# Optimization experiments

Measured on AMD Instinct MI355X. Metric: run time of the kernel, lower is better.

The kernel has to match this reference:

```python
import jax, jax.numpy as jnp
import numpy as np

B, S, D, V, H, L = 2, 64, 1024, 32000, 8, 2
HD = D // H

def setup_inputs():
    key = jax.random.key(0)
    ks = jax.random.split(key, 12)
    w = lambda k, shp: jax.random.normal(k, shp, jnp.float32) * 0.02
    return {
        "embedded_answer": jax.random.normal(ks[0], (B, S, D), jnp.float32),
        "sa_in_w": w(ks[1], (L, 3 * D, D)), "sa_in_b": jnp.zeros((L, 3 * D), jnp.float32),
        "sa_out_w": w(ks[2], (L, D, D)), "sa_out_b": jnp.zeros((L, D), jnp.float32),
        "ca_in_w": w(ks[3], (L, 3 * D, D)), "ca_in_b": jnp.zeros((L, 3 * D), jnp.float32),
        "ca_out_w": w(ks[4], (L, D, D)), "ca_out_b": jnp.zeros((L, D), jnp.float32),
        "ff1_w": w(ks[5], (L, 4 * D, D)), "ff1_b": jnp.zeros((L, 4 * D), jnp.float32),
        "ff2_w": w(ks[6], (L, D, 4 * D)), "ff2_b": jnp.zeros((L, D), jnp.float32),
        "ln_w": jnp.ones((L, 3, D), jnp.float32), "ln_b": jnp.zeros((L, 3, D), jnp.float32),
        "out_w": w(ks[7], (V, D)), "out_b": jnp.zeros((V,), jnp.float32),
        "temp_w": w(ks[8], (1, D)), "temp_b": jnp.zeros((1,), jnp.float32),
        "len_w": w(ks[9], (1, D)), "len_b": jnp.zeros((1,), jnp.float32),
        "style_w": w(ks[10], (D, D)), "style_b": jnp.zeros((D,), jnp.float32),
        "num_steps": 8,
    }

def _ln(x, w, b, eps=1e-5):
    m = x.mean(-1, keepdims=True)
    v = ((x - m) ** 2).mean(-1, keepdims=True)
    return (x - m) * jax.lax.rsqrt(v + eps) * w + b

def _mha(q_in, kv_in, in_w, in_b, ow, ob):
    wq, wk, wv = jnp.split(in_w, 3, 0)
    bq, bk, bv = jnp.split(in_b, 3, 0)
    q = (q_in @ wq.T + bq).reshape(q_in.shape[0], q_in.shape[1], H, HD)
    k = (kv_in @ wk.T + bk).reshape(kv_in.shape[0], kv_in.shape[1], H, HD)
    v = (kv_in @ wv.T + bv).reshape(kv_in.shape[0], kv_in.shape[1], H, HD)
    a = jax.nn.softmax(jnp.einsum('bqhd,bkhd->bhqk', q, k) * (HD ** -0.5), axis=-1)
    o = jnp.einsum('bhqk,bkhd->bqhd', a, v).reshape(q_in.shape)
    return o @ ow.T + ob

def _decode(x, mem, l, p):
    # post-LN torch TransformerDecoderLayer (relu FFN, no masks, eval/no dropout)
    x = _ln(x + _mha(x, x, p['sa_in_w'][l], p['sa_in_b'][l], p['sa_out_w'][l], p['sa_out_b'][l]), p['ln_w'][l, 0], p['ln_b'][l, 0])
    x = _ln(x + _mha(x, mem, p['ca_in_w'][l], p['ca_in_b'][l], p['ca_out_w'][l], p['ca_out_b'][l]), p['ln_w'][l, 1], p['ln_b'][l, 1])
    h = jax.nn.relu(x @ p['ff1_w'][l].T + p['ff1_b'][l]) @ p['ff2_w'][l].T + p['ff2_b'][l]
    return _ln(x + h, p['ln_w'][l, 2], p['ln_b'][l, 2])

def reference(embedded_answer, sa_in_w, sa_in_b, sa_out_w, sa_out_b, ca_in_w, ca_in_b, ca_out_w, ca_out_b, ff1_w, ff1_b, ff2_w, ff2_b, ln_w, ln_b, out_w, out_b, temp_w, temp_b, len_w, len_b, style_w, style_b, num_steps):
    p = dict(sa_in_w=sa_in_w, sa_in_b=sa_in_b, sa_out_w=sa_out_w, sa_out_b=sa_out_b,
             ca_in_w=ca_in_w, ca_in_b=ca_in_b, ca_out_w=ca_out_w, ca_out_b=ca_out_b,
             ff1_w=ff1_w, ff1_b=ff1_b, ff2_w=ff2_w, ff2_b=ff2_b, ln_w=ln_w, ln_b=ln_b)
    # control_generation (per-batch mean temperature / mean style vector)
    temp = jax.nn.sigmoid(embedded_answer @ temp_w.T + temp_b).mean(axis=(1, 2))[:, None]  # [B,1]
    _length_factor = jax.nn.sigmoid(embedded_answer @ len_w.T + len_b)  # drives static num_steps
    style = (embedded_answer @ style_w.T + style_b).mean(axis=1, keepdims=True)  # [B,1,D]
    cur = embedded_answer
    skey = jax.random.key(42)
    toks, lgs = [], []
    for t in range(num_steps):  # static unrolled decode loop; full recompute (no KV cache), as original
        h = cur
        for l in range(L):
            h = _decode(h, embedded_answer, l, p)
        logits_last = ((h + style)[:, -1, :] @ out_w.T + out_b) / temp  # [B,V]
        nt = jax.random.categorical(jax.random.fold_in(skey, t), logits_last)  # == softmax+multinomial
        toks.append(nt)
        lgs.append(logits_last)
        cur = jnp.concatenate([cur, out_w[nt][:, None, :]], axis=1)  # re-embed via output weight rows
    return jnp.stack(toks, 1), jnp.stack(lgs, 1)
```

## Files before the change

kernel.cpp:

```cpp
#include <hip/hip_runtime.h>
#include <stdint.h>

__host__ __device__ inline void threefry2x32(uint32_t k0, uint32_t k1,
                                             uint32_t x0, uint32_t x1,
                                             uint32_t* o0, uint32_t* o1) {
  uint32_t ks2 = 0x1BD11BDAu ^ k0 ^ k1;
  x0 += k0; x1 += k1;
#define TF_R(x, r) (((x) << (r)) | ((x) >> (32 - (r))))
#define TF_ROUND(r) { x0 += x1; x1 = TF_R(x1, r); x1 ^= x0; }
  TF_ROUND(13) TF_ROUND(15) TF_ROUND(26) TF_ROUND(6)
  x0 += k1; x1 += ks2 + 1u;
  TF_ROUND(17) TF_ROUND(29) TF_ROUND(16) TF_ROUND(24)
  x0 += ks2; x1 += k0 + 2u;
  TF_ROUND(13) TF_ROUND(15) TF_ROUND(26) TF_ROUND(6)
  x0 += k0; x1 += k1 + 3u;
  TF_ROUND(17) TF_ROUND(29) TF_ROUND(16) TF_ROUND(24)
  x0 += k1; x1 += ks2 + 4u;
  TF_ROUND(13) TF_ROUND(15) TF_ROUND(26) TF_ROUND(6)
  x0 += ks2; x1 += k0 + 5u;
  *o0 = x0; *o1 = x1;
#undef TF_ROUND
#undef TF_R
}

__device__ __forceinline__ float wave_sum(float v) {
#pragma unroll
  for (int o = 32; o > 0; o >>= 1) v += __shfl_xor(v, o, 64);
  return v;
}
__device__ __forceinline__ float wave_max(float v) {
#pragma unroll
  for (int o = 32; o > 0; o >>= 1) v = fmaxf(v, __shfl_xor(v, o, 64));
  return v;
}

__global__ __launch_bounds__(256) void gemm2_kernel(
    const float* __restrict__ X, long long xbs, int ldx,
    const float* __restrict__ W, int ldw,
    const float* __restrict__ bias,
    float* __restrict__ out, long long obs, int ldo,
    int St, int M, int N, int K32, int relu, int partial) {
  __shared__ __align__(16) float Xl[2][32][68];
  __shared__ __align__(16) float Wl[2][32][68];
  const int tid = threadIdx.x;
  const int m0 = blockIdx.x * 64;
  const int n0 = blockIdx.y * 64;
  const long long kbase = (long long)blockIdx.z * K32 * 32;
  const int mi = tid >> 4;
  const int ni = tid & 15;
  const int lr = tid >> 3;
  const int lc = (tid & 7) * 4;

  const int mA = m0 + lr, mB = m0 + lr + 32;
  const float* xpA = nullptr;
  const float* xpB = nullptr;
  if (mA < M) {
    int b = mA / St, s = mA - b * St;
    xpA = X + (long long)b * xbs + (long long)s * ldx + kbase + lc;
  }
  if (mB < M) {
    int b = mB / St, s = mB - b * St;
    xpB = X + (long long)b * xbs + (long long)s * ldx + kbase + lc;
  }
  const float* wpA = W + (long long)(n0 + lr) * ldw + kbase + lc;
  const float* wpB = W + (long long)(n0 + lr + 32) * ldw + kbase + lc;

  float4 xA = xpA ? *(const float4*)xpA : make_float4(0.f, 0.f, 0.f, 0.f);
  float4 xB = xpB ? *(const float4*)xpB : make_float4(0.f, 0.f, 0.f, 0.f);
  float4 wA = *(const float4*)wpA;
  float4 wB = *(const float4*)wpB;

  float acc[4][4];
#pragma unroll
  for (int i = 0; i < 4; ++i)
#pragma unroll
    for (int j = 0; j < 4; ++j) acc[i][j] = 0.f;

  Xl[0][lc + 0][lr] = xA.x; Xl[0][lc + 1][lr] = xA.y;
  Xl[0][lc + 2][lr] = xA.z; Xl[0][lc + 3][lr] = xA.w;
  Xl[0][lc + 0][lr + 32] = xB.x; Xl[0][lc + 1][lr + 32] = xB.y;
  Xl[0][lc + 2][lr + 32] = xB.z; Xl[0][lc + 3][lr + 32] = xB.w;
  Wl[0][lc + 0][lr] = wA.x; Wl[0][lc + 1][lr] = wA.y;
  Wl[0][lc + 2][lr] = wA.z; Wl[0][lc + 3][lr] = wA.w;
  Wl[0][lc + 0][lr + 32] = wB.x; Wl[0][lc + 1][lr + 32] = wB.y;
  Wl[0][lc + 2][lr + 32] = wB.z; Wl[0][lc + 3][lr + 32] = wB.w;
  __syncthreads();

  for (int i = 0; i < K32; ++i) {
    if (i + 1 < K32) {
      int off = (i + 1) * 32;
      xA = xpA ? *(const float4*)(xpA + off) : make_float4(0.f, 0.f, 0.f, 0.f);
      xB = xpB ? *(const float4*)(xpB + off) : make_float4(0.f, 0.f, 0.f, 0.f);
      wA = *(const float4*)(wpA + off);
      wB = *(const float4*)(wpB + off);
    }
    const int cur = i & 1;
#pragma unroll
    for (int kk = 0; kk < 32; ++kk) {
      float4 xv = *(const float4*)&Xl[cur][kk][mi * 4];
      float4 wv = *(const float4*)&Wl[cur][kk][ni * 4];
      float xa[4] = {xv.x, xv.y, xv.z, xv.w};
      float wa[4] = {wv.x, wv.y, wv.z, wv.w};
#pragma unroll
      for (int a = 0; a < 4; ++a)
#pragma unroll
        for (int c = 0; c < 4; ++c) acc[a][c] = fmaf(xa[a], wa[c], acc[a][c]);
    }
    if (i + 1 < K32) {
      __syncthreads();
      const int nxt = cur ^ 1;
      Xl[nxt][lc + 0][lr] = xA.x; Xl[nxt][lc + 1][lr] = xA.y;
      Xl[nxt][lc + 2][lr] = xA.z; Xl[nxt][lc + 3][lr] = xA.w;
      Xl[nxt][lc + 0][lr + 32] = xB.x; Xl[nxt][lc + 1][lr + 32] = xB.y;
      Xl[nxt][lc + 2][lr + 32] = xB.z; Xl[nxt][lc + 3][lr + 32] = xB.w;
      Wl[nxt][lc + 0][lr] = wA.x; Wl[nxt][lc + 1][lr] = wA.y;
      Wl[nxt][lc + 2][lr] = wA.z; Wl[nxt][lc + 3][lr] = wA.w;
      Wl[nxt][lc + 0][lr + 32] = wB.x; Wl[nxt][lc + 1][lr + 32] = wB.y;
      Wl[nxt][lc + 2][lr + 32] = wB.z; Wl[nxt][lc + 3][lr + 32] = wB.w;
      __syncthreads();
    }
  }

  const int n = n0 + ni * 4;
  if (partial) {
    float* base = out + (long long)blockIdx.z * M * ldo;
#pragma unroll
    for (int i = 0; i < 4; ++i) {
      int m = m0 + mi * 4 + i;
      if (m >= M) continue;
      *(float4*)(base + (long long)m * ldo + n) =
          make_float4(acc[i][0], acc[i][1], acc[i][2], acc[i][3]);
    }
  } else {
    float4 bv = *(const float4*)(bias + n);
#pragma unroll
    for (int i = 0; i < 4; ++i) {
      int m = m0 + mi * 4 + i;
      if (m >= M) continue;
      int b = m / St, s = m - b * St;
      float4 o;
      o.x = acc[i][0] + bv.x; o.y = acc[i][1] + bv.y;
      o.z = acc[i][2] + bv.z; o.w = acc[i][3] + bv.w;
      if (relu) {
        o.x = fmaxf(o.x, 0.f); o.y = fmaxf(o.y, 0.f);
        o.z = fmaxf(o.z, 0.f); o.w = fmaxf(o.w, 0.f);
      }
      *(float4*)(out + (long long)b * obs + (long long)s * ldo + n) = o;
    }
  }
}

__global__ __launch_bounds__(256) void epi_kernel(
    const float* __restrict__ P, int splits, int M, int N,
    const float* __restrict__ bias,
    const float* __restrict__ res, long long rbs, int ldr,
    const float* __restrict__ lnw, const float* __restrict__ lnb,
    float* __restrict__ out, long long obs, int ldo, int St, int relu) {
  __shared__ float red[4];
  const int m = blockIdx.x;
  const int b = m / St, s = m - b * St;
  const int n = blockIdx.y * 1024 + threadIdx.x * 4;
  const float* pr = P + (long long)m * N + n;
  float4 v = *(const float4*)pr;
  for (int sp = 1; sp < splits; ++sp) {
    float4 w2 = *(const float4*)(pr + (long long)sp * M * N);
    v.x += w2.x; v.y += w2.y; v.z += w2.z; v.w += w2.w;
  }
  float4 bv = *(const float4*)(bias + n);
  v.x += bv.x; v.y += bv.y; v.z += bv.z; v.w += bv.w;
  if (res) {
    float4 rv = *(const float4*)(res + (long long)b * rbs + (long long)s * ldr + n);
    v.x += rv.x; v.y += rv.y; v.z += rv.z; v.w += rv.w;
  }
  if (relu) {
    v.x = fmaxf(v.x, 0.f); v.y = fmaxf(v.y, 0.f);
    v.z = fmaxf(v.z, 0.f); v.w = fmaxf(v.w, 0.f);
  }
  if (lnw) {
    const int tid = threadIdx.x;
    float sum = wave_sum(v.x + v.y + v.z + v.w);
    int wid = tid >> 6;
    if ((tid & 63) == 0) red[wid] = sum;
    __syncthreads();
    float mean = (red[0] + red[1] + red[2] + red[3]) * (1.f / 1024.f);
    float4 d;
    d.x = v.x - mean; d.y = v.y - mean; d.z = v.z - mean; d.w = v.w - mean;
    float s2 = wave_sum(d.x * d.x + d.y * d.y + d.z * d.z + d.w * d.w);
    __syncthreads();
    if ((tid & 63) == 0) red[wid] = s2;
    __syncthreads();
    float var = (red[0] + red[1] + red[2] + red[3]) * (1.f / 1024.f);
    float inv = rsqrtf(var + 1e-5f);
    float4 wv = *(const float4*)(lnw + tid * 4);
    float4 lb = *(const float4*)(lnb + tid * 4);
    v.x = d.x * inv * wv.x + lb.x;
    v.y = d.y * inv * wv.y + lb.y;
    v.z = d.z * inv * wv.z + lb.z;
    v.w = d.w * inv * wv.w + lb.w;
  }
  *(float4*)(out + (long long)b * obs + (long long)s * ldo + n) = v;
}

__global__ __launch_bounds__(64) void attn_kernel(
    const float* __restrict__ Qp, int q_rs, long long q_bs,
    const float* __restrict__ Kp, int k_rs, long long k_bs,
    const float* __restrict__ Vp, int v_rs, long long v_bs,
    float* __restrict__ Op, int o_rs, long long o_bs,
    int Sq, int Skv) {
  const int lane = threadIdx.x;
  int bid = blockIdx.x;
  int b = bid / (8 * Sq);
  int rr = bid - b * 8 * Sq;
  int h = rr / Sq;
  int sq = rr - h * Sq;
  const float* qrow = Qp + (long long)b * q_bs + (long long)sq * q_rs + h * 128;
  float q0 = qrow[lane], q1 = qrow[lane + 64];
  __shared__ float sc[72];
  const float* kb = Kp + (long long)b * k_bs + h * 128;
  for (int sk = 0; sk < Skv; ++sk) {
    const float* kr = kb + (long long)sk * k_rs;
    float p = fmaf(q0, kr[lane], q1 * kr[lane + 64]);
    p = wave_sum(p);
    if (lane == 0) sc[sk] = p * 0.08838834764831845f;
  }
  __syncthreads();
  float m = -3.4e38f;
  for (int i = lane; i < Skv; i += 64) m = fmaxf(m, sc[i]);
  m = wave_max(m);
  float ssum = 0.f;
  for (int i = lane; i < Skv; i += 64) {
    float e = expf(sc[i] - m);
    sc[i] = e;
    ssum += e;
  }
  ssum = wave_sum(ssum);
  __syncthreads();
  float o0 = 0.f, o1 = 0.f;
  const float* vb = Vp + (long long)b * v_bs + h * 128;
  for (int sk = 0; sk < Skv; ++sk) {
    float w = sc[sk];
    const float* vr = vb + (long long)sk * v_rs;
    o0 = fmaf(w, vr[lane], o0);
    o1 = fmaf(w, vr[lane + 64], o1);
  }
  float inv = 1.f / ssum;
  float* orow = Op + (long long)b * o_bs + (long long)sq * o_rs + h * 128;
  orow[lane] = o0 * inv;
  orow[lane + 64] = o1 * inv;
}

__global__ __launch_bounds__(256) void copy_cur_kernel(
    const float* __restrict__ emb, float* __restrict__ cur) {
  int idx = blockIdx.x * 256 + threadIdx.x;
  int b = idx >> 16;
  int r = idx & 65535;
  cur[(long long)b * 73728 + r] = emb[idx];
}

__global__ __launch_bounds__(256) void xmean_kernel(
    const float* __restrict__ emb, float* __restrict__ xmean) {
  int idx = blockIdx.x * 256 + threadIdx.x;
  int b = idx >> 10, d = idx & 1023;
  float s = 0.f;
  for (int ss = 0; ss < 64; ++ss) s += emb[b * 65536 + ss * 1024 + d];
  xmean[idx] = s * (1.f / 64.f);
}

__global__ __launch_bounds__(256) void temp_kernel(
    const float* __restrict__ emb, const float* __restrict__ tw,
    const float* __restrict__ tb, float* __restrict__ tempv) {
  __shared__ float red[4];
  int b = blockIdx.x;
  int wid = threadIdx.x >> 6, lane = threadIdx.x & 63;
  float acc = 0.f;
  for (int s = wid; s < 64; s += 4) {
    const float* x = emb + b * 65536 + s * 1024;
    float p = 0.f;
#pragma unroll
    for (int it = 0; it < 4; ++it) {
      float4 xv = *(const float4*)(x + it * 256 + lane * 4);
      float4 wv = *(const float4*)(tw + it * 256 + lane * 4);
      p += xv.x * wv.x + xv.y * wv.y + xv.z * wv.z + xv.w * wv.w;
    }
    p = wave_sum(p);
    acc += 1.f / (1.f + expf(-(p + tb[0])));
  }
  if (lane == 0) red[wid] = acc;
  __syncthreads();
  if (threadIdx.x == 0)
    tempv[b] = (red[0] + red[1] + red[2] + red[3]) * (1.f / 64.f);
}

__global__ __launch_bounds__(256) void style_kernel(
    const float* __restrict__ xmean, const float* __restrict__ sw,
    const float* __restrict__ sb, float* __restrict__ stylev) {
  int wid = threadIdx.x >> 6, lane = threadIdx.x & 63;
  int d = blockIdx.x * 4 + wid;
  const float* wr = sw + (long long)d * 1024;
  float a0 = 0.f, a1 = 0.f;
#pragma unroll
  for (int it = 0; it < 4; ++it) {
    float4 wv = *(const float4*)(wr + it * 256 + lane * 4);
    float4 x0 = *(const float4*)(xmean + it * 256 + lane * 4);
    float4 x1 = *(const float4*)(xmean + 1024 + it * 256 + lane * 4);
    a0 += wv.x * x0.x + wv.y * x0.y + wv.z * x0.z + wv.w * x0.w;
    a1 += wv.x * x1.x + wv.y * x1.y + wv.z * x1.z + wv.w * x1.w;
  }
  a0 = wave_sum(a0);
  a1 = wave_sum(a1);
  if (lane == 0) {
    stylev[d] = a0 + sb[d];
    stylev[1024 + d] = a1 + sb[d];
  }
}

__global__ __launch_bounds__(256) void z_kernel(
    const float* __restrict__ A, const float* __restrict__ stylev,
    float* __restrict__ z, int St) {
  int idx = blockIdx.x * 256 + threadIdx.x;
  int b = idx >> 10, d = idx & 1023;
  z[idx] = A[(long long)b * 73728 + (long long)(St - 1) * 1024 + d] + stylev[idx];
}

__global__ __launch_bounds__(256) void logits_kernel(
    const float* __restrict__ z, const float* __restrict__ Wo,
    const float* __restrict__ bo, const float* __restrict__ tempv,
    float* __restrict__ outl, int t) {
  int wid = threadIdx.x >> 6, lane = threadIdx.x & 63;
  int n = blockIdx.x * 4 + wid;
  const float* wr = Wo + (long long)n * 1024;
  float a0 = 0.f, a1 = 0.f;
#pragma unroll
  for (int it = 0; it < 4; ++it) {
    float4 wv = *(const float4*)(wr + it * 256 + lane * 4);
    float4 z0 = *(const float4*)(z + it * 256 + lane * 4);
    float4 z1 = *(const float4*)(z + 1024 + it * 256 + lane * 4);
    a0 += wv.x * z0.x + wv.y * z0.y + wv.z * z0.z + wv.w * z0.w;
    a1 += wv.x * z1.x + wv.y * z1.y + wv.z * z1.z + wv.w * z1.w;
  }
  a0 = wave_sum(a0);
  a1 = wave_sum(a1);
  if (lane == 0) {
    float bb = bo[n];
    outl[(long long)(0 * 8 + t) * 32000 + n] = (a0 + bb) / tempv[0];
    outl[(long long)(1 * 8 + t) * 32000 + n] = (a1 + bb) / tempv[1];
  }
}

__global__ __launch_bounds__(1024) void sample_kernel(
    const float* __restrict__ logits, float* __restrict__ tok_f,
    int* __restrict__ tok_i, uint32_t fk0, uint32_t fk1, int t) {
  int b = blockIdx.x;
  const float* lg = logits + (long long)(b * 8 + t) * 32000;
  float best = -3.4e38f;
  int bi = 0x7fffffff;
  for (int n = threadIdx.x; n < 32000; n += 1024) {
    uint32_t r0, r1;
    threefry2x32(fk0, fk1, 0u, (uint32_t)(b * 32000 + n), &r0, &r1);
    uint32_t bits = (r0 ^ r1) >> 9;
    float u = __uint_as_float(0x3f800000u | bits) - 1.0f;
    if (u < 1.1754944e-38f) u = 1.1754944e-38f;
    float g = -logf(-logf(u));
    float val = lg[n] + g;
    if (val > best) { best = val; bi = n; }
  }
  __shared__ float bv[1024];
  __shared__ int bix[1024];
  bv[threadIdx.x] = best;
  bix[threadIdx.x] = bi;
  __syncthreads();
  for (int s = 512; s > 0; s >>= 1) {
    if (threadIdx.x < s) {
      float ov = bv[threadIdx.x + s];
      int oi = bix[threadIdx.x + s];
      if (ov > bv[threadIdx.x] ||
          (ov == bv[threadIdx.x] && oi < bix[threadIdx.x])) {
        bv[threadIdx.x] = ov;
        bix[threadIdx.x] = oi;
      }
    }
    __syncthreads();
  }
  if (threadIdx.x == 0) {
    tok_i[b] = bix[0];
    tok_f[b * 8 + t] = (float)bix[0];
  }
}

__global__ __launch_bounds__(256) void append_kernel(
    const float* __restrict__ Wo, const int* __restrict__ tok_i,
    float* __restrict__ cur, int St) {
  int idx = blockIdx.x * 256 + threadIdx.x;
  int b = idx >> 10, d = idx & 1023;
  cur[(long long)b * 73728 + (long long)St * 1024 + d] =
      Wo[(long long)tok_i[b] * 1024 + d];
}

static inline void g2(hipStream_t st, const float* X, long long xbs, int ldx,
                      const float* W, int ldw, const float* bias, float* out,
                      long long obs, int ldo, int St, int M, int N, int K,
                      int splits, int relu, int partial) {
  dim3 grid((unsigned)((M + 63) / 64), (unsigned)(N / 64), (unsigned)splits);
  gemm2_kernel<<<grid, 256, 0, st>>>(X, xbs, ldx, W, ldw, bias, out, obs, ldo,
                                     St, M, N, K / (32 * splits), relu,
                                     partial);
}

static inline void epi(hipStream_t st, const float* P, int splits, int M,
                       int N, const float* bias, const float* res,
                       long long rbs, int ldr, const float* lnw,
                       const float* lnb, float* out, long long obs, int ldo,
                       int St, int relu) {
  dim3 grid((unsigned)M, (unsigned)(N / 1024));
  epi_kernel<<<grid, 256, 0, st>>>(P, splits, M, N, bias, res, rbs, ldr, lnw,
                                   lnb, out, obs, ldo, St, relu);
}

extern "C" void kernel_launch(void* const* d_in, const int* in_sizes, int n_in,
                              void* d_out, int out_size, void* d_ws,
                              size_t ws_size, hipStream_t stream) {
  const float* emb = (const float*)d_in[0];
  const float* sa_in_w = (const float*)d_in[1];
  const float* sa_in_b = (const float*)d_in[2];
  const float* sa_out_w = (const float*)d_in[3];
  const float* sa_out_b = (const float*)d_in[4];
  const float* ca_in_w = (const float*)d_in[5];
  const float* ca_in_b = (const float*)d_in[6];
  const float* ca_out_w = (const float*)d_in[7];
  const float* ca_out_b = (const float*)d_in[8];
  const float* ff1_w = (const float*)d_in[9];
  const float* ff1_b = (const float*)d_in[10];
  const float* ff2_w = (const float*)d_in[11];
  const float* ff2_b = (const float*)d_in[12];
  const float* ln_w = (const float*)d_in[13];
  const float* ln_b = (const float*)d_in[14];
  const float* out_w = (const float*)d_in[15];
  const float* out_b = (const float*)d_in[16];
  const float* temp_w = (const float*)d_in[17];
  const float* temp_b = (const float*)d_in[18];
  const float* style_w = (const float*)d_in[21];
  const float* style_b = (const float*)d_in[22];

  float* ws = (float*)d_ws;
  float* cur = ws;
  float* A = cur + 2 * 72 * 1024;
  float* Qb = A + 2 * 72 * 1024;
  float* Tb = Qb + 2 * 72 * 3072;
  float* T2 = Tb + 2 * 72 * 1024;
  float* Fb = T2 + 2 * 72 * 1024;
  float* cakv = Fb + 2 * 72 * 4096;
  float* Pp = cakv + 2 * 2 * 64 * 2048;
  float* xmean = Pp + 1310720;
  float* stylev = xmean + 2048;
  float* tempv = stylev + 2048;
  float* zbuf = tempv + 16;
  int* toki = (int*)(zbuf + 2048);

  float* toks_out = (float*)d_out;
  float* logits_out = toks_out + 16;

  copy_cur_kernel<<<512, 256, 0, stream>>>(emb, cur);
  xmean_kernel<<<8, 256, 0, stream>>>(emb, xmean);
  temp_kernel<<<2, 256, 0, stream>>>(emb, temp_w, temp_b, tempv);
  style_kernel<<<256, 256, 0, stream>>>(xmean, style_w, style_b, stylev);
  for (int l = 0; l < 2; ++l) {
    g2(stream, emb, 64 * 1024, 1024,
       ca_in_w + (size_t)(l * 3072 + 1024) * 1024, 1024,
       ca_in_b + l * 3072 + 1024, cakv + (size_t)l * 2 * 64 * 2048, 64 * 2048,
       2048, 64, 128, 2048, 1024, 1, 0, 0);
  }

  for (int t = 0; t < 8; ++t) {
    int St = 64 + t;
    int M = 2 * St;
    for (int l = 0; l < 2; ++l) {
      const float* P0 = (l == 0) ? cur : A;
      g2(stream, P0, 72 * 1024, 1024, sa_in_w + (size_t)l * 3072 * 1024, 1024,
         nullptr, Pp, 0, 3072, St, M, 3072, 1024, 2, 0, 1);
      epi(stream, Pp, 2, M, 3072, sa_in_b + l * 3072, nullptr, 0, 0, nullptr,
          nullptr, Qb, 72 * 3072, 3072, St, 0);
      attn_kernel<<<2 * 8 * St, 64, 0, stream>>>(
          Qb, 3072, 72 * 3072, Qb + 1024, 3072, 72 * 3072, Qb + 2048, 3072,
          72 * 3072, Tb, 1024, 72 * 1024, St, St);
      g2(stream, Tb, 72 * 1024, 1024, sa_out_w + (size_t)l * 1024 * 1024, 1024,
         nullptr, Pp, 0, 1024, St, M, 1024, 1024, 4, 0, 1);
      epi(stream, Pp, 4, M, 1024, sa_out_b + l * 1024, P0, 72 * 1024, 1024,
          ln_w + (l * 3 + 0) * 1024, ln_b + (l * 3 + 0) * 1024, A, 72 * 1024,
          1024, St, 0);
      g2(stream, A, 72 * 1024, 1024, ca_in_w + (size_t)l * 3072 * 1024, 1024,
         nullptr, Pp, 0, 1024, St, M, 1024, 1024, 4, 0, 1);
      epi(stream, Pp, 4, M, 1024, ca_in_b + l * 3072, nullptr, 0, 0, nullptr,
          nullptr, T2, 72 * 1024, 1024, St, 0);
      attn_kernel<<<2 * 8 * St, 64, 0, stream>>>(
          T2, 1024, 72 * 1024, cakv + (size_t)l * 2 * 64 * 2048, 2048,
          64 * 2048, cakv + (size_t)l * 2 * 64 * 2048 + 1024, 2048, 64 * 2048,
          Tb, 1024, 72 * 1024, St, 64);
      g2(stream, Tb, 72 * 1024, 1024, ca_out_w + (size_t)l * 1024 * 1024, 1024,
         nullptr, Pp, 0, 1024, St, M, 1024, 1024, 4, 0, 1);
      epi(stream, Pp, 4, M, 1024, ca_out_b + l * 1024, A, 72 * 1024, 1024,
          ln_w + (l * 3 + 1) * 1024, ln_b + (l * 3 + 1) * 1024, A, 72 * 1024,
          1024, St, 0);
      g2(stream, A, 72 * 1024, 1024, ff1_w + (size_t)l * 4096 * 1024, 1024,
         nullptr, Pp, 0, 4096, St, M, 4096, 1024, 2, 0, 1);
      epi(stream, Pp, 2, M, 4096, ff1_b + l * 4096, nullptr, 0, 0, nullptr,
          nullptr, Fb, 72 * 4096, 4096, St, 1);
      g2(stream, Fb, 72 * 4096, 4096, ff2_w + (size_t)l * 1024 * 4096, 4096,
         nullptr, Pp, 0, 1024, St, M, 1024, 4096, 8, 0, 1);
      epi(stream, Pp, 8, M, 1024, ff2_b + l * 1024, A, 72 * 1024, 1024,
          ln_w + (l * 3 + 2) * 1024, ln_b + (l * 3 + 2) * 1024, A, 72 * 1024,
          1024, St, 0);
    }
    z_kernel<<<8, 256, 0, stream>>>(A, stylev, zbuf, St);
    logits_kernel<<<8000, 256, 0, stream>>>(zbuf, out_w, out_b, tempv,
                                            logits_out, t);
    uint32_t fk0, fk1;
    threefry2x32(0u, 42u, 0u, (uint32_t)t, &fk0, &fk1);
    sample_kernel<<<2, 1024, 0, stream>>>(logits_out, toks_out, toki, fk0, fk1,
                                          t);
    append_kernel<<<8, 256, 0, stream>>>(out_w, toki, cur, St);
  }
}
```

Baseline: 5.627 ms.

## Fuse epilogues into GEMMs, attention, logits and sampling to cut launches

Removes separate epilogue launches. The QKV and FF1 projections now run unsplit and write bias (and ReLU) directly from the GEMM, and the cross-attention Q projection uses a 2-way split whose two partials plus bias are summed inside the attention kernel. The z kernel is folded into the logits kernel, and the token-append kernel is folded into the sampling kernel. This cuts roughly 5 launches per layer-step and some intermediate traffic, at the cost of less split-K parallelism for the unsplit GEMMs.

```diff
diff --git a/kernel.cpp b/kernel.cpp
--- a/kernel.cpp
+++ b/kernel.cpp
@@ -203,6 +203,8 @@
 
 __global__ __launch_bounds__(64) void attn_kernel(
     const float* __restrict__ Qp, int q_rs, long long q_bs,
+    const float* __restrict__ Qp2,
+    const float* __restrict__ qbias,
     const float* __restrict__ Kp, int k_rs, long long k_bs,
     const float* __restrict__ Vp, int v_rs, long long v_bs,
     float* __restrict__ Op, int o_rs, long long o_bs,
@@ -215,6 +217,13 @@
   int sq = rr - h * Sq;
   const float* qrow = Qp + (long long)b * q_bs + (long long)sq * q_rs + h * 128;
   float q0 = qrow[lane], q1 = qrow[lane + 64];
+  if (Qp2) {
+    const float* q2 = Qp2 + (long long)b * q_bs + (long long)sq * q_rs + h * 128;
+    q0 += q2[lane]; q1 += q2[lane + 64];
+  }
+  if (qbias) {
+    q0 += qbias[h * 128 + lane]; q1 += qbias[h * 128 + lane + 64];
+  }
   __shared__ float sc[72];
   const float* kb = Kp + (long long)b * k_bs + h * 128;
   for (int sk = 0; sk < Skv; ++sk) {
@@ -314,27 +323,26 @@
   }
 }
 
-__global__ __launch_bounds__(256) void z_kernel(
-    const float* __restrict__ A, const float* __restrict__ stylev,
-    float* __restrict__ z, int St) {
-  int idx = blockIdx.x * 256 + threadIdx.x;
-  int b = idx >> 10, d = idx & 1023;
-  z[idx] = A[(long long)b * 73728 + (long long)(St - 1) * 1024 + d] + stylev[idx];
-}
-
 __global__ __launch_bounds__(256) void logits_kernel(
-    const float* __restrict__ z, const float* __restrict__ Wo,
-    const float* __restrict__ bo, const float* __restrict__ tempv,
-    float* __restrict__ outl, int t) {
+    const float* __restrict__ A, const float* __restrict__ stylev, int St,
+    const float* __restrict__ Wo, const float* __restrict__ bo,
+    const float* __restrict__ tempv, float* __restrict__ outl, int t) {
   int wid = threadIdx.x >> 6, lane = threadIdx.x & 63;
   int n = blockIdx.x * 4 + wid;
   const float* wr = Wo + (long long)n * 1024;
+  const float* a0p = A + (long long)(St - 1) * 1024;
+  const float* a1p = A + 73728 + (long long)(St - 1) * 1024;
   float a0 = 0.f, a1 = 0.f;
 #pragma unroll
   for (int it = 0; it < 4; ++it) {
-    float4 wv = *(const float4*)(wr + it * 256 + lane * 4);
-    float4 z0 = *(const float4*)(z + it * 256 + lane * 4);
-    float4 z1 = *(const float4*)(z + 1024 + it * 256 + lane * 4);
+    int off = it * 256 + lane * 4;
+    float4 wv = *(const float4*)(wr + off);
+    float4 x0 = *(const float4*)(a0p + off);
+    float4 s0 = *(const float4*)(stylev + off);
+    float4 x1 = *(const float4*)(a1p + off);
+    float4 s1 = *(const float4*)(stylev + 1024 + off);
+    float4 z0 = make_float4(x0.x + s0.x, x0.y + s0.y, x0.z + s0.z, x0.w + s0.w);
+    float4 z1 = make_float4(x1.x + s1.x, x1.y + s1.y, x1.z + s1.z, x1.w + s1.w);
     a0 += wv.x * z0.x + wv.y * z0.y + wv.z * z0.z + wv.w * z0.w;
     a1 += wv.x * z1.x + wv.y * z1.y + wv.z * z1.z + wv.w * z1.w;
   }
@@ -348,8 +356,9 @@
 }
 
 __global__ __launch_bounds__(1024) void sample_kernel(
-    const float* __restrict__ logits, float* __restrict__ tok_f,
-    int* __restrict__ tok_i, uint32_t fk0, uint32_t fk1, int t) {
+    const float* __restrict__ logits, const float* __restrict__ Wo,
+    float* __restrict__ tok_f, float* __restrict__ cur, int St,
+    uint32_t fk0, uint32_t fk1, int t) {
   int b = blockIdx.x;
   const float* lg = logits + (long long)(b * 8 + t) * 32000;
   float best = -3.4e38f;
@@ -381,19 +390,10 @@
     }
     __syncthreads();
   }
-  if (threadIdx.x == 0) {
-    tok_i[b] = bix[0];
-    tok_f[b * 8 + t] = (float)bix[0];
-  }
-}
-
-__global__ __launch_bounds__(256) void append_kernel(
-    const float* __restrict__ Wo, const int* __restrict__ tok_i,
-    float* __restrict__ cur, int St) {
-  int idx = blockIdx.x * 256 + threadIdx.x;
-  int b = idx >> 10, d = idx & 1023;
-  cur[(long long)b * 73728 + (long long)St * 1024 + d] =
-      Wo[(long long)tok_i[b] * 1024 + d];
+  int tok = bix[0];
+  if (threadIdx.x == 0) tok_f[b * 8 + t] = (float)tok;
+  cur[(long long)b * 73728 + (long long)St * 1024 + threadIdx.x] =
+      Wo[(long long)tok * 1024 + threadIdx.x];
 }
 
 static inline void g2(hipStream_t st, const float* X, long long xbs, int ldx,
@@ -446,15 +446,12 @@
   float* A = cur + 2 * 72 * 1024;
   float* Qb = A + 2 * 72 * 1024;
   float* Tb = Qb + 2 * 72 * 3072;
-  float* T2 = Tb + 2 * 72 * 1024;
-  float* Fb = T2 + 2 * 72 * 1024;
+  float* Fb = Tb + 2 * 72 * 1024;
   float* cakv = Fb + 2 * 72 * 4096;
   float* Pp = cakv + 2 * 2 * 64 * 2048;
   float* xmean = Pp + 1310720;
   float* stylev = xmean + 2048;
   float* tempv = stylev + 2048;
-  float* zbuf = tempv + 16;
-  int* toki = (int*)(zbuf + 2048);
 
   float* toks_out = (float*)d_out;
   float* logits_out = toks_out + 16;
@@ -476,23 +473,20 @@
     for (int l = 0; l < 2; ++l) {
       const float* P0 = (l == 0) ? cur : A;
       g2(stream, P0, 72 * 1024, 1024, sa_in_w + (size_t)l * 3072 * 1024, 1024,
-         nullptr, Pp, 0, 3072, St, M, 3072, 1024, 2, 0, 1);
-      epi(stream, Pp, 2, M, 3072, sa_in_b + l * 3072, nullptr, 0, 0, nullptr,
-          nullptr, Qb, 72 * 3072, 3072, St, 0);
+         sa_in_b + l * 3072, Qb, 72 * 3072, 3072, St, M, 3072, 1024, 1, 0, 0);
       attn_kernel<<<2 * 8 * St, 64, 0, stream>>>(
-          Qb, 3072, 72 * 3072, Qb + 1024, 3072, 72 * 3072, Qb + 2048, 3072,
-          72 * 3072, Tb, 1024, 72 * 1024, St, St);
+          Qb, 3072, 72 * 3072, nullptr, nullptr, Qb + 1024, 3072, 72 * 3072,
+          Qb + 2048, 3072, 72 * 3072, Tb, 1024, 72 * 1024, St, St);
       g2(stream, Tb, 72 * 1024, 1024, sa_out_w + (size_t)l * 1024 * 1024, 1024,
          nullptr, Pp, 0, 1024, St, M, 1024, 1024, 4, 0, 1);
       epi(stream, Pp, 4, M, 1024, sa_out_b + l * 1024, P0, 72 * 1024, 1024,
           ln_w + (l * 3 + 0) * 1024, ln_b + (l * 3 + 0) * 1024, A, 72 * 1024,
           1024, St, 0);
       g2(stream, A, 72 * 1024, 1024, ca_in_w + (size_t)l * 3072 * 1024, 1024,
-         nullptr, Pp, 0, 1024, St, M, 1024, 1024, 4, 0, 1);
-      epi(stream, Pp, 4, M, 1024, ca_in_b + l * 3072, nullptr, 0, 0, nullptr,
-          nullptr, T2, 72 * 1024, 1024, St, 0);
+         nullptr, Pp, 0, 1024, St, M, 1024, 1024, 2, 0, 1);
       attn_kernel<<<2 * 8 * St, 64, 0, stream>>>(
-          T2, 1024, 72 * 1024, cakv + (size_t)l * 2 * 64 * 2048, 2048,
+          Pp, 1024, (long long)St * 1024, Pp + (size_t)M * 1024,
+          ca_in_b + l * 3072, cakv + (size_t)l * 2 * 64 * 2048, 2048,
           64 * 2048, cakv + (size_t)l * 2 * 64 * 2048 + 1024, 2048, 64 * 2048,
           Tb, 1024, 72 * 1024, St, 64);
       g2(stream, Tb, 72 * 1024, 1024, ca_out_w + (size_t)l * 1024 * 1024, 1024,
@@ -501,22 +495,18 @@
           ln_w + (l * 3 + 1) * 1024, ln_b + (l * 3 + 1) * 1024, A, 72 * 1024,
           1024, St, 0);
       g2(stream, A, 72 * 1024, 1024, ff1_w + (size_t)l * 4096 * 1024, 1024,
-         nullptr, Pp, 0, 4096, St, M, 4096, 1024, 2, 0, 1);
-      epi(stream, Pp, 2, M, 4096, ff1_b + l * 4096, nullptr, 0, 0, nullptr,
-          nullptr, Fb, 72 * 4096, 4096, St, 1);
+         ff1_b + l * 4096, Fb, 72 * 4096, 4096, St, M, 4096, 1024, 1, 1, 0);
       g2(stream, Fb, 72 * 4096, 4096, ff2_w + (size_t)l * 1024 * 4096, 4096,
          nullptr, Pp, 0, 1024, St, M, 1024, 4096, 8, 0, 1);
       epi(stream, Pp, 8, M, 1024, ff2_b + l * 1024, A, 72 * 1024, 1024,
           ln_w + (l * 3 + 2) * 1024, ln_b + (l * 3 + 2) * 1024, A, 72 * 1024,
           1024, St, 0);
     }
-    z_kernel<<<8, 256, 0, stream>>>(A, stylev, zbuf, St);
-    logits_kernel<<<8000, 256, 0, stream>>>(zbuf, out_w, out_b, tempv,
-                                            logits_out, t);
+    logits_kernel<<<8000, 256, 0, stream>>>(A, stylev, St, out_w, out_b,
+                                            tempv, logits_out, t);
     uint32_t fk0, fk1;
     threefry2x32(0u, 42u, 0u, (uint32_t)t, &fk0, &fk1);
-    sample_kernel<<<2, 1024, 0, stream>>>(logits_out, toks_out, toki, fk0, fk1,
-                                          t);
-    append_kernel<<<8, 256, 0, stream>>>(out_w, toki, cur, St);
-  }
-}
+    sample_kernel<<<2, 1024, 0, stream>>>(logits_out, out_w, toks_out, cur,
+                                          St, fk0, fk1, t);
+  }
+}
```

New measurement: 5.834 ms. 3.7% more time.
